# Kernel tuning notes

Measured on AMD Instinct MI355X. Metric: run time of the kernel, lower is better.

The kernel has to match this reference:

```python
import jax, jax.numpy as jnp
import numpy as np

WIN = (8, 8)
NUM_HEADS = 6


def bchw_to_bnc(x, win):
    B, C, H, W = x.shape
    SH, SW = win
    oh, ow = H // SH, W // SW
    # B,C,oh,SH,ow,SW -> B,oh,ow,SH,SW,C -> (B*oh*ow, SH*SW, C)
    x = x.reshape(B, C, oh, SH, ow, SW)
    x = jnp.transpose(x, (0, 2, 4, 3, 5, 1))
    return x.reshape(B * oh * ow, SH * SW, C)


def bnc_to_bchw(x, out_shape, win):
    OB, OC, OH, OW = out_shape
    SH, SW = win
    oh, ow = OH // SH, OW // SW
    C = x.shape[-1]
    x = x.reshape(OB, oh, ow, SH, SW, C)
    x = jnp.transpose(x, (0, 5, 1, 3, 2, 4))
    return x.reshape(OB, C, OH, OW)


def setup_inputs() -> dict:
    key = jax.random.key(0)
    k1, k2, k3 = jax.random.split(key, 3)
    B, C, H, W = 4, 192, 384, 384
    x = jax.random.normal(k1, (B, C, H, W), dtype=jnp.float32)
    # MHA params: qkv_proj Linear(C, 3C), head_proj Linear(C, C)
    qkv_w = jax.random.normal(k2, (3 * C, C), dtype=jnp.float32) * 0.02
    qkv_b = jnp.zeros((3 * C,), dtype=jnp.float32)
    head_w = jax.random.normal(k3, (C, C), dtype=jnp.float32) * 0.02
    head_b = jnp.zeros((C,), dtype=jnp.float32)
    return {"x": x, "qkv_w": qkv_w, "qkv_b": qkv_b, "head_w": head_w, "head_b": head_b}


def reference(x, qkv_w, qkv_b, head_w, head_b):
    out_shape = x.shape
    C = x.shape[1]
    H = NUM_HEADS
    D = C // H  # head dim
    # window partition: (Bw, N, C) with N = 64
    t = bchw_to_bnc(x, WIN)
    # QKV projection
    qkv = t @ qkv_w.T + qkv_b  # (Bw, N, 3C)
    q, k, v = jnp.split(qkv, 3, axis=-1)
    Bw, N, _ = q.shape
    q = q.reshape(Bw, N, H, D).transpose(0, 2, 1, 3)  # bhnd
    k = k.reshape(Bw, N, H, D).transpose(0, 2, 1, 3)
    v = v.reshape(Bw, N, H, D).transpose(0, 2, 1, 3)
    scale = 1.0 / jnp.sqrt(jnp.asarray(D, dtype=q.dtype))
    scores = jnp.einsum('bhqd,bhkd->bhqk', q, k) * scale
    attn = jax.nn.softmax(scores, axis=-1)
    o = jnp.einsum('bhqk,bhkd->bhqd', attn, v)
    o = o.transpose(0, 2, 1, 3).reshape(Bw, N, C)
    o = o @ head_w.T + head_b
    return bnc_to_bchw(o, out_shape, WIN)
```

## Files before the change

### kernel.cpp

```cpp
#include <hip/hip_runtime.h>
#include <hip/hip_bf16.h>

typedef __attribute__((ext_vector_type(8))) short short8;
typedef __attribute__((ext_vector_type(4))) float f32x4;

#if __has_builtin(__builtin_amdgcn_exp2f)
#define EXP2F(x) __builtin_amdgcn_exp2f(x)
#else
#define EXP2F(x) exp2f(x)
#endif
#if __has_builtin(__builtin_amdgcn_rcpf)
#define RCPF(x) __builtin_amdgcn_rcpf(x)
#else
#define RCPF(x) (1.0f/(x))
#endif

#define SQ 208
#define SV 144

#define LDS_TOTAL 62976

__device__ __forceinline__ unsigned short f2bf(float f) {
    union { float f; unsigned u; } v; v.f = f;
    unsigned r = v.u + 0x7FFFu + ((v.u >> 16) & 1u);
    return (unsigned short)(r >> 16);
}
__device__ __forceinline__ unsigned pk2(float lo, float hi) {
    __hip_bfloat162 h = __float22bfloat162_rn(make_float2(lo, hi));
    union { __hip_bfloat162 h; unsigned u; } cv;
    cv.h = h;
    return cv.u;
}

__global__ void cvt_weights(const float* __restrict__ qw, const float* __restrict__ hw,
                            unsigned short* __restrict__ wq, unsigned short* __restrict__ wh) {
    int i = blockIdx.x * 256 + threadIdx.x;
    if (i < 576 * 192) wq[i] = f2bf(qw[i]);
    if (i < 192 * 192) wh[i] = f2bf(hw[i]);
}

__global__ __launch_bounds__(256, 2) void wmha(
    const float* __restrict__ x, const float* __restrict__ qkv_b,
    const float* __restrict__ head_b, const unsigned short* __restrict__ wq,
    const unsigned short* __restrict__ whc, float* __restrict__ out)
{
    extern __shared__ char smem[];
    char* const x_lds = smem;
    char* const q_lds = smem;
    char* const k_lds = smem + 13312;
    char* const v_lds = smem + 26624;
    char* const o_lds = smem + 40448;

    const int tid = threadIdx.x;
    const int ln  = tid & 15;
    const int hi4 = (tid >> 4) & 3;
    const int wid = tid >> 6;
    char* const p_scr = smem + 53760 + wid * 2304;

    const int bid  = blockIdx.x;
    const int widx = (bid & 7) * 1152 + (bid >> 3);
    const int b  = widx / 2304;
    const int rr = widx % 2304;
    const int oy = rr / 48, ox = rr % 48;
    const int row0 = oy * 8, col0 = ox * 8;

    {
        const int tok = tid & 63;
        const int qd  = tid >> 6;
        const int y = tok >> 3, xx = tok & 7;
        const float* gp = x + ((size_t)(b * 192) * 384 + (row0 + y)) * 384 + (col0 + xx);
        char* wp = x_lds + tok * 400 + qd * 96;
        #pragma unroll
        for (int kk = 0; kk < 12; ++kk) {
            const int c = qd * 48 + kk * 4;
            float f0 = gp[(size_t)(c + 0) * 147456];
            float f1 = gp[(size_t)(c + 1) * 147456];
            float f2 = gp[(size_t)(c + 2) * 147456];
            float f3 = gp[(size_t)(c + 3) * 147456];
            uint2 u;
            u.x = pk2(f0, f1);
            u.y = pk2(f2, f3);
            *(uint2*)(wp + kk * 8) = u;
        }
    }
    __syncthreads();

    short8 bx[4][6];
    #pragma unroll
    for (int nt = 0; nt < 4; ++nt)
        #pragma unroll
        for (int kt = 0; kt < 6; ++kt)
            bx[nt][kt] = *(const short8*)(x_lds + (nt * 16 + ln) * 400 + kt * 64 + hi4 * 16);
    __syncthreads();

    f32x4 acc[3][4];
    #pragma unroll
    for (int mm = 0; mm < 3; ++mm)
        #pragma unroll
        for (int nt = 0; nt < 4; ++nt)
            acc[mm][nt] = (f32x4){0.f, 0.f, 0.f, 0.f};

    const float SC2 = 0.25503417f;

    auto qkv = [&](int g) {
        for (int mt = wid; mt < 18; mt += 4) {
            const int hl = mt / 6, sec = (mt % 6) >> 1, e = mt & 1;
            const int r0 = sec * 192 + (3 * g + hl) * 32 + e * 16;
            short8 wf[6];
            #pragma unroll
            for (int kt = 0; kt < 6; ++kt)
                wf[kt] = *(const short8*)(wq + (r0 + ln) * 192 + kt * 32 + hi4 * 8);
            if (sec < 2) {
                char* dst = (sec == 0) ? q_lds : k_lds;
                const float4 bias = *(const float4*)(qkv_b + r0 + hi4 * 4);
                #pragma unroll
                for (int nt = 0; nt < 4; ++nt) {
                    f32x4 a = {bias.x, bias.y, bias.z, bias.w};
                    #pragma unroll
                    for (int kt = 0; kt < 6; ++kt)
                        a = __builtin_amdgcn_mfma_f32_16x16x32_bf16(wf[kt], bx[nt][kt], a, 0, 0, 0);
                    uint2 u;
                    u.x = pk2(a[0], a[1]);
                    u.y = pk2(a[2], a[3]);
                    *(uint2*)(dst + (nt * 16 + ln) * SQ + hl * 64 + (e * 16 + hi4 * 4) * 2) = u;
                }
            } else {
                const float bv = qkv_b[r0 + ln];
                #pragma unroll
                for (int nt = 0; nt < 4; ++nt) {
                    f32x4 a = {bv, bv, bv, bv};
                    #pragma unroll
                    for (int kt = 0; kt < 6; ++kt)
                        a = __builtin_amdgcn_mfma_f32_16x16x32_bf16(bx[nt][kt], wf[kt], a, 0, 0, 0);
                    uint2 u;
                    u.x = pk2(a[0], a[1]);
                    u.y = pk2(a[2], a[3]);
                    *(uint2*)(v_lds + (hl * 32 + e * 16 + ln) * SV + (nt * 16 + hi4 * 4) * 2) = u;
                }
            }
        }
    };

    auto attn = [&](int g) {
        #pragma unroll
        for (int uu = 0; uu < 3; ++uu) {
            const int u = wid + uu * 4;
            const int hl = u >> 2, i0 = (u & 3) * 16;
            const short8 bq = *(const short8*)(q_lds + (i0 + ln) * SQ + hl * 64 + hi4 * 16);
            f32x4 s[4];
            #pragma unroll
            for (int kt = 0; kt < 4; ++kt) {
                const short8 ak = *(const short8*)(k_lds + (kt * 16 + ln) * SQ + hl * 64 + hi4 * 16);
                f32x4 z = {0.f, 0.f, 0.f, 0.f};
                s[kt] = __builtin_amdgcn_mfma_f32_16x16x32_bf16(ak, bq, z, 0, 0, 0);
            }
            float m = s[0][0];
            #pragma unroll
            for (int kt = 0; kt < 4; ++kt)
                #pragma unroll
                for (int r = 0; r < 4; ++r) m = fmaxf(m, s[kt][r]);
            m = fmaxf(m, __shfl_xor(m, 16));
            m = fmaxf(m, __shfl_xor(m, 32));
            float sum = 0.f;
            #pragma unroll
            for (int kt = 0; kt < 4; ++kt)
                #pragma unroll
                for (int r = 0; r < 4; ++r) {
                    s[kt][r] = EXP2F((s[kt][r] - m) * SC2);
                    sum += s[kt][r];
                }
            sum += __shfl_xor(sum, 16);
            sum += __shfl_xor(sum, 32);
            const float rinv = RCPF(sum);
            #pragma unroll
            for (int kt = 0; kt < 4; ++kt) {
                uint2 u2;
                u2.x = pk2(s[kt][0], s[kt][1]);
                u2.y = pk2(s[kt][2], s[kt][3]);
                *(uint2*)(p_scr + ln * SV + kt * 32 + hi4 * 8) = u2;
            }
            short8 pf[2];
            #pragma unroll
            for (int kc = 0; kc < 2; ++kc)
                pf[kc] = *(const short8*)(p_scr + ln * SV + kc * 64 + hi4 * 16);
            #pragma unroll
            for (int dt = 0; dt < 2; ++dt) {
                f32x4 o = {0.f, 0.f, 0.f, 0.f};
                #pragma unroll
                for (int kc = 0; kc < 2; ++kc) {
                    const short8 av = *(const short8*)(v_lds + (hl * 32 + dt * 16 + ln) * SV + kc * 64 + hi4 * 16);
                    o = __builtin_amdgcn_mfma_f32_16x16x32_bf16(av, pf[kc], o, 0, 0, 0);
                }
                uint2 u2;
                u2.x = pk2(o[0] * rinv, o[1] * rinv);
                u2.y = pk2(o[2] * rinv, o[3] * rinv);
                *(uint2*)(o_lds + (i0 + ln) * SQ + hl * 64 + (dt * 16 + hi4 * 4) * 2) = u2;
            }
        }
    };

    auto proj = [&](int g) {
        short8 bo[4][3];
        #pragma unroll
        for (int nt = 0; nt < 4; ++nt)
            #pragma unroll
            for (int kt = 0; kt < 3; ++kt)
                bo[nt][kt] = *(const short8*)(o_lds + (nt * 16 + ln) * SQ + kt * 64 + hi4 * 16);
        #pragma unroll
        for (int mm = 0; mm < 3; ++mm) {
            const int c0 = (wid * 3 + mm) * 16;
            short8 af[3];
            #pragma unroll
            for (int kt = 0; kt < 3; ++kt)
                af[kt] = *(const short8*)(whc + (c0 + ln) * 192 + g * 96 + kt * 32 + hi4 * 8);
            #pragma unroll
            for (int nt = 0; nt < 4; ++nt)
                #pragma unroll
                for (int kt = 0; kt < 3; ++kt)
                    acc[mm][nt] = __builtin_amdgcn_mfma_f32_16x16x32_bf16(af[kt], bo[nt][kt], acc[mm][nt], 0, 0, 0);
        }
    };

    qkv(0);
    __syncthreads();
    attn(0);
    __syncthreads();
    proj(0);
    qkv(1);
    __syncthreads();
    attn(1);
    __syncthreads();
    proj(1);

    #pragma unroll
    for (int mm = 0; mm < 3; ++mm) {
        const int c0 = (wid * 3 + mm) * 16;
        const float4 hb = *(const float4*)(head_b + c0 + hi4 * 4);
        #pragma unroll
        for (int nt = 0; nt < 4; ++nt) {
            const int tt = nt * 16 + ln;
            const int y = tt >> 3, xx = tt & 7;
            float* op = out + ((size_t)(b * 192) * 384 + (row0 + y)) * 384 + (col0 + xx);
            op[(size_t)(c0 + hi4 * 4 + 0) * 147456] = acc[mm][nt][0] + hb.x;
            op[(size_t)(c0 + hi4 * 4 + 1) * 147456] = acc[mm][nt][1] + hb.y;
            op[(size_t)(c0 + hi4 * 4 + 2) * 147456] = acc[mm][nt][2] + hb.z;
            op[(size_t)(c0 + hi4 * 4 + 3) * 147456] = acc[mm][nt][3] + hb.w;
        }
    }
}

extern "C" void kernel_launch(void* const* d_in, const int* in_sizes, int n_in,
                              void* d_out, int out_size, void* d_ws, size_t ws_size,
                              hipStream_t stream) {
    const float* x      = (const float*)d_in[0];
    const float* qkv_w  = (const float*)d_in[1];
    const float* qkv_b  = (const float*)d_in[2];
    const float* head_w = (const float*)d_in[3];
    const float* head_b = (const float*)d_in[4];
    float* out = (float*)d_out;

    unsigned short* wq  = (unsigned short*)d_ws;
    unsigned short* whc = wq + 576 * 192;

    cvt_weights<<<432, 256, 0, stream>>>(qkv_w, head_w, wq, whc);

    hipFuncSetAttribute((const void*)wmha, hipFuncAttributeMaxDynamicSharedMemorySize, LDS_TOTAL);
    wmha<<<9216, 256, LDS_TOTAL, stream>>>(x, qkv_b, head_b, wq, whc, out);
}
```

Measured before the change: 560.2 us.

## Fuse head projection into attention via register shuffles, drop o_lds round trip

Each wave now owns a 16-token row block across all heads, and the attention output fragment is rearranged with cross-lane shuffles into an MFMA B operand. That operand feeds the head projection directly, accumulating into 12 per-wave output tiles. This removes the O staging in LDS, the separate proj phase and two barriers, and moves q/k/v out of the x buffer so the post-load sync can go. The cost is more LDS (which may reduce occupancy at 2 blocks per CU), more accumulator registers, and head weights reloaded per head iteration.

Result: slower. 736.1 us (+31.4%).

```diff
diff --git a/kernel.cpp b/kernel.cpp
--- a/kernel.cpp
+++ b/kernel.cpp
@@ -18,7 +18,7 @@
 #define SQ 208
 #define SV 144
 
-#define LDS_TOTAL 62976
+#define LDS_TOTAL 75264
 
 __device__ __forceinline__ unsigned short f2bf(float f) {
     union { float f; unsigned u; } v; v.f = f;
@@ -46,16 +46,15 @@
 {
     extern __shared__ char smem[];
     char* const x_lds = smem;
-    char* const q_lds = smem;
-    char* const k_lds = smem + 13312;
-    char* const v_lds = smem + 26624;
-    char* const o_lds = smem + 40448;
+    char* const q_lds = smem + 25600;
+    char* const k_lds = smem + 38912;
+    char* const v_lds = smem + 52224;
 
     const int tid = threadIdx.x;
     const int ln  = tid & 15;
     const int hi4 = (tid >> 4) & 3;
     const int wid = tid >> 6;
-    char* const p_scr = smem + 53760 + wid * 2304;
+    char* const p_scr = smem + 66048 + wid * 2304;
 
     const int bid  = blockIdx.x;
     const int widx = (bid & 7) * 1152 + (bid >> 3);
@@ -91,14 +90,8 @@
         #pragma unroll
         for (int kt = 0; kt < 6; ++kt)
             bx[nt][kt] = *(const short8*)(x_lds + (nt * 16 + ln) * 400 + kt * 64 + hi4 * 16);
-    __syncthreads();
-
-    f32x4 acc[3][4];
-    #pragma unroll
-    for (int mm = 0; mm < 3; ++mm)
-        #pragma unroll
-        for (int nt = 0; nt < 4; ++nt)
-            acc[mm][nt] = (f32x4){0.f, 0.f, 0.f, 0.f};
+
+    f32x4 acc[12];
 
     const float SC2 = 0.25503417f;
 
@@ -144,8 +137,8 @@
     auto attn = [&](int g) {
         #pragma unroll
         for (int uu = 0; uu < 3; ++uu) {
-            const int u = wid + uu * 4;
-            const int hl = u >> 2, i0 = (u & 3) * 16;
+            const int hl = uu;
+            const int i0 = wid * 16;
             const short8 bq = *(const short8*)(q_lds + (i0 + ln) * SQ + hl * 64 + hi4 * 16);
             f32x4 s[4];
             #pragma unroll
@@ -183,6 +176,7 @@
             #pragma unroll
             for (int kc = 0; kc < 2; ++kc)
                 pf[kc] = *(const short8*)(p_scr + ln * SV + kc * 64 + hi4 * 16);
+            f32x4 of[2];
             #pragma unroll
             for (int dt = 0; dt < 2; ++dt) {
                 f32x4 o = {0.f, 0.f, 0.f, 0.f};
@@ -191,60 +185,58 @@
                     const short8 av = *(const short8*)(v_lds + (hl * 32 + dt * 16 + ln) * SV + kc * 64 + hi4 * 16);
                     o = __builtin_amdgcn_mfma_f32_16x16x32_bf16(av, pf[kc], o, 0, 0, 0);
                 }
-                uint2 u2;
-                u2.x = pk2(o[0] * rinv, o[1] * rinv);
-                u2.y = pk2(o[2] * rinv, o[3] * rinv);
-                *(uint2*)(o_lds + (i0 + ln) * SQ + hl * 64 + (dt * 16 + hi4 * 4) * 2) = u2;
+                of[dt] = o;
+            }
+            unsigned pko[2][2];
+            #pragma unroll
+            for (int dt = 0; dt < 2; ++dt) {
+                pko[dt][0] = pk2(of[dt][0] * rinv, of[dt][1] * rinv);
+                pko[dt][1] = pk2(of[dt][2] * rinv, of[dt][3] * rinv);
+            }
+            const int h = hi4;
+            const bool hiH = (h >= 2);
+            unsigned F[2], S[2];
+            #pragma unroll
+            for (int rp = 0; rp < 2; ++rp) {
+                unsigned pub16 = hiH ? pko[1][rp] : pko[0][rp];
+                unsigned pub3x = (h < 2) ? pko[1][rp] : pko[0][rp];
+                unsigned r16 = __shfl_xor(pub16, 16);
+                unsigned r32 = __shfl_xor(pub3x, 32);
+                unsigned r48 = __shfl_xor(pub3x, 48);
+                F[rp] = (h == 0) ? pko[0][rp] : (h == 1) ? r48 : (h == 2) ? r32 : r16;
+                S[rp] = (h == 3) ? pko[1][rp] : (h == 2) ? r48 : (h == 1) ? r32 : r16;
+            }
+            union { uint4 u4; short8 s8; } cv;
+            cv.u4.x = F[0]; cv.u4.y = F[1]; cv.u4.z = S[0]; cv.u4.w = S[1];
+            const short8 bo = cv.s8;
+            #pragma unroll
+            for (int mm = 0; mm < 12; ++mm) {
+                const short8 af = *(const short8*)(whc + (mm * 16 + ln) * 192 + g * 96 + hl * 32 + hi4 * 8);
+                f32x4 cin = (g == 0 && uu == 0) ? (f32x4){0.f, 0.f, 0.f, 0.f} : acc[mm];
+                acc[mm] = __builtin_amdgcn_mfma_f32_16x16x32_bf16(af, bo, cin, 0, 0, 0);
             }
         }
     };
 
-    auto proj = [&](int g) {
-        short8 bo[4][3];
-        #pragma unroll
-        for (int nt = 0; nt < 4; ++nt)
-            #pragma unroll
-            for (int kt = 0; kt < 3; ++kt)
-                bo[nt][kt] = *(const short8*)(o_lds + (nt * 16 + ln) * SQ + kt * 64 + hi4 * 16);
-        #pragma unroll
-        for (int mm = 0; mm < 3; ++mm) {
-            const int c0 = (wid * 3 + mm) * 16;
-            short8 af[3];
-            #pragma unroll
-            for (int kt = 0; kt < 3; ++kt)
-                af[kt] = *(const short8*)(whc + (c0 + ln) * 192 + g * 96 + kt * 32 + hi4 * 8);
-            #pragma unroll
-            for (int nt = 0; nt < 4; ++nt)
-                #pragma unroll
-                for (int kt = 0; kt < 3; ++kt)
-                    acc[mm][nt] = __builtin_amdgcn_mfma_f32_16x16x32_bf16(af[kt], bo[nt][kt], acc[mm][nt], 0, 0, 0);
-        }
-    };
-
     qkv(0);
     __syncthreads();
     attn(0);
     __syncthreads();
-    proj(0);
     qkv(1);
     __syncthreads();
     attn(1);
-    __syncthreads();
-    proj(1);
-
-    #pragma unroll
-    for (int mm = 0; mm < 3; ++mm) {
-        const int c0 = (wid * 3 + mm) * 16;
-        const float4 hb = *(const float4*)(head_b + c0 + hi4 * 4);
-        #pragma unroll
-        for (int nt = 0; nt < 4; ++nt) {
-            const int tt = nt * 16 + ln;
-            const int y = tt >> 3, xx = tt & 7;
-            float* op = out + ((size_t)(b * 192) * 384 + (row0 + y)) * 384 + (col0 + xx);
-            op[(size_t)(c0 + hi4 * 4 + 0) * 147456] = acc[mm][nt][0] + hb.x;
-            op[(size_t)(c0 + hi4 * 4 + 1) * 147456] = acc[mm][nt][1] + hb.y;
-            op[(size_t)(c0 + hi4 * 4 + 2) * 147456] = acc[mm][nt][2] + hb.z;
-            op[(size_t)(c0 + hi4 * 4 + 3) * 147456] = acc[mm][nt][3] + hb.w;
+
+    {
+        const int t = wid * 16 + ln;
+        const int y = t >> 3, xx = t & 7;
+        #pragma unroll
+        for (int mm = 0; mm < 12; ++mm) {
+            const float4 hb = *(const float4*)(head_b + mm * 16 + hi4 * 4);
+            float* op = out + ((size_t)(b * 192 + mm * 16 + hi4 * 4) * 384 + (row0 + y)) * 384 + (col0 + xx);
+            op[0]          = acc[mm][0] + hb.x;
+            op[147456]     = acc[mm][1] + hb.y;
+            op[2 * 147456] = acc[mm][2] + hb.z;
+            op[3 * 147456] = acc[mm][3] + hb.w;
         }
     }
 }
```
